# Performance work log

Hardware: AMD Instinct MI355X
Metric: run time of the kernel (lower is better)

Reference implementation:

```python
import jax, jax.numpy as jnp
import numpy as np

EMBED = 256
HEADS = 8
HD = EMBED // HEADS          # head_dim = key_dim = 32 (value_factor=1)
SCALE = HD ** (-0.5)


def angle_transform(x, sin, cos):
    # x: (b, nh, h, w, hd); sin/cos broadcast over leading dims
    x1 = x[..., ::2]
    x2 = x[..., 1::2]
    rot = jnp.stack([-x2, x1], axis=-1).reshape(x.shape)  # interleave (-x2, x1)
    return x * cos + rot * sin


def setup_inputs() -> dict:
    key = jax.random.key(0)
    ks = jax.random.split(key, 12)
    B, H, W = 4, 48, 48
    x = jax.random.normal(ks[0], (B, H, W, EMBED), jnp.float32)
    ang = jax.random.normal(ks[1], (H, W, HD), jnp.float32)
    sin = jnp.sin(ang)
    cos = jnp.cos(ang)
    mask = jax.random.normal(ks[2], (HEADS, H * W, H * W), jnp.float32) * 0.1
    s = 0.05
    Wq = jax.random.normal(ks[3], (EMBED, EMBED), jnp.float32) * s
    bq = jnp.zeros((EMBED,), jnp.float32)
    Wk = jax.random.normal(ks[4], (EMBED, EMBED), jnp.float32) * s
    bk = jnp.zeros((EMBED,), jnp.float32)
    Wv = jax.random.normal(ks[5], (EMBED, EMBED), jnp.float32) * s
    bv = jnp.zeros((EMBED,), jnp.float32)
    lepe_w = jax.random.normal(ks[6], (5, 5, 1, EMBED), jnp.float32) * 0.1  # HWIO, depthwise
    lepe_b = jnp.zeros((EMBED,), jnp.float32)
    Wout = jax.random.normal(ks[7], (EMBED, EMBED), jnp.float32) * s
    bout = jnp.zeros((EMBED,), jnp.float32)
    return {"x": x, "sin": sin, "cos": cos, "mask": mask,
            "Wq": Wq, "bq": bq, "Wk": Wk, "bk": bk, "Wv": Wv, "bv": bv,
            "lepe_w": lepe_w, "lepe_b": lepe_b, "Wout": Wout, "bout": bout}


def reference(x, sin, cos, mask, Wq, bq, Wk, bk, Wv, bv, lepe_w, lepe_b, Wout, bout):
    B, H, W, C = x.shape
    q = x @ Wq + bq
    k = (x @ Wk + bk) * SCALE
    v = x @ Wv + bv
    # depthwise 5x5 conv (lepe) on v, NHWC
    lepe = jax.lax.conv_general_dilated(
        v, lepe_w, window_strides=(1, 1), padding=[(2, 2), (2, 2)],
        dimension_numbers=("NHWC", "HWIO", "NHWC"), feature_group_count=C) + lepe_b
    qh = q.reshape(B, H, W, HEADS, HD).transpose(0, 3, 1, 2, 4)  # (b,nh,h,w,hd)
    kh = k.reshape(B, H, W, HEADS, HD).transpose(0, 3, 1, 2, 4)
    qr = angle_transform(qh, sin, cos).reshape(B, HEADS, H * W, HD)
    kr = angle_transform(kh, sin, cos).reshape(B, HEADS, H * W, HD)
    vr = v.reshape(B, H, W, HEADS, -1).transpose(0, 3, 1, 2, 4).reshape(B, HEADS, H * W, -1)
    attn = jax.nn.softmax(jnp.einsum("bnqd,bnkd->bnqk", qr, kr) + mask, axis=-1)
    out = jnp.einsum("bnqk,bnkd->bnqd", attn, vr)
    out = out.transpose(0, 2, 1, 3).reshape(B, H, W, -1) + lepe
    return out @ Wout + bout
```

## Files before the change

kernel.cpp:

```cpp
#include <hip/hip_runtime.h>
#include <hip/hip_bf16.h>
#include <math.h>

constexpr int kB     = 4;
constexpr int kH     = 48;
constexpr int kW     = 48;
constexpr int kHW    = 2304;
constexpr int kC     = 256;
constexpr int kHeads = 8;
constexpr int kHD    = 32;
constexpr float kScale = 0.17677669529663687f;

typedef __bf16 bf16x8 __attribute__((ext_vector_type(8)));
typedef float  f32x4  __attribute__((ext_vector_type(4)));
typedef unsigned int   uint32x4 __attribute__((ext_vector_type(4)));
typedef unsigned short ushort8v __attribute__((ext_vector_type(8)));

static __device__ __forceinline__ unsigned short f2bf_bits(float f) {
    return __builtin_bit_cast(unsigned short, __float2bfloat16(f));
}

static __device__ __forceinline__ unsigned cvt_pk_bf16(float lo, float hi) {
    unsigned r;
    asm("v_cvt_pk_bf16_f32 %0, %1, %2" : "=v"(r) : "v"(lo), "v"(hi));
    return r;
}

static __device__ __forceinline__ void gll16(const void* g, void* l) {
    __builtin_amdgcn_global_load_lds(
        (const __attribute__((address_space(1))) void*)g,
        (__attribute__((address_space(3))) void*)l, 16, 0, 0);
}

__global__ __launch_bounds__(256) void prep_kernel(
    const float* __restrict__ x,
    const float* __restrict__ Wq, const float* __restrict__ Wk,
    const float* __restrict__ Wv, const float* __restrict__ Wo,
    unsigned short* __restrict__ xb, unsigned short* __restrict__ wt)
{
    const int bid = blockIdx.x;
    if (bid < 2304) {
        const int i = (bid * 256 + threadIdx.x) * 4;
        const float4 v = *reinterpret_cast<const float4*>(x + i);
        alignas(8) unsigned short u[4] = {f2bf_bits(v.x), f2bf_bits(v.y),
                                          f2bf_bits(v.z), f2bf_bits(v.w)};
        *reinterpret_cast<unsigned long long*>(xb + i) =
            *reinterpret_cast<unsigned long long*>(u);
    } else {
        const int e = (bid - 2304) * 256 + threadIdx.x;
        const int m = e >> 16;
        const int r = e & 65535;
        const int k = r >> 8;
        const int n = r & 255;
        const float* W = (m == 0) ? Wq : ((m == 1) ? Wk : ((m == 2) ? Wv : Wo));
        wt[(size_t)m * 65536 + n * 256 + k] = f2bf_bits(W[k * 256 + n]);
    }
}

__global__ __launch_bounds__(256) void qkv_mfma_kernel(
    const unsigned short* __restrict__ xb, const unsigned short* __restrict__ wt,
    const float* __restrict__ bq, const float* __restrict__ bk,
    const float* __restrict__ bv,
    const float* __restrict__ sinb, const float* __restrict__ cosb,
    unsigned short* __restrict__ qbh, unsigned short* __restrict__ kbh,
    unsigned short* __restrict__ vt, float* __restrict__ vb)
{
    const int z = blockIdx.z;
    const unsigned short* wz = wt + (size_t)z * 65536;
    const float* bt = (z == 0) ? bq : ((z == 1) ? bk : bv);
    const int tid  = threadIdx.x;
    const int w    = tid >> 6;
    const int lane = tid & 63;
    const int l    = lane & 15;
    const int g    = lane >> 4;
    const int m0   = blockIdx.x * 64 + w * 16;
    const int nb   = blockIdx.y * 64;

    f32x4 acc[4] = {};
    const unsigned short* xrow = xb + (size_t)(m0 + l) * 256;
    #pragma unroll
    for (int kc = 0; kc < 8; ++kc) {
        const bf16x8 a = *reinterpret_cast<const bf16x8*>(xrow + kc * 32 + g * 8);
        #pragma unroll
        for (int j = 0; j < 4; ++j) {
            const bf16x8 b = *reinterpret_cast<const bf16x8*>(
                wz + (size_t)(nb + 16 * j + l) * 256 + kc * 32 + g * 8);
            acc[j] = __builtin_amdgcn_mfma_f32_16x16x32_bf16(a, b, acc[j], 0, 0, 0);
        }
    }

    int tok[4], bidx[4], hw[4];
    #pragma unroll
    for (int r = 0; r < 4; ++r) {
        tok[r]  = m0 + 4 * g + r;
        bidx[r] = tok[r] / kHW;
        hw[r]   = tok[r] - bidx[r] * kHW;
    }
    const float scl = (z == 1) ? kScale : 1.0f;

    if (z == 2) {
        #pragma unroll
        for (int j = 0; j < 4; ++j) {
            const int c = nb + 16 * j + l;
            const int head = c >> 5, d = c & 31;
            const float bias = bt[c];
            float t[4];
            #pragma unroll
            for (int r = 0; r < 4; ++r) t[r] = acc[j][r] + bias;
            #pragma unroll
            for (int r = 0; r < 4; ++r)
                vb[(((size_t)(bidx[r] * kHeads + head) * kHW + hw[r]) << 5) + d] = t[r];
            alignas(8) unsigned short u[4] = {f2bf_bits(t[0]), f2bf_bits(t[1]),
                                              f2bf_bits(t[2]), f2bf_bits(t[3])};
            *reinterpret_cast<unsigned long long*>(
                vt + ((size_t)(bidx[0] * kHeads + head) * kHD + d) * kHW + hw[0]) =
                *reinterpret_cast<unsigned long long*>(u);
        }
    } else {
        unsigned short* ob = (z == 0) ? qbh : kbh;
        #pragma unroll
        for (int j = 0; j < 4; ++j) {
            const int c = nb + 16 * j + l;
            const int head = c >> 5, d = c & 31;
            const float bias = bt[c];
            float t[4];
            #pragma unroll
            for (int r = 0; r < 4; ++r) t[r] = (acc[j][r] + bias) * scl;
            #pragma unroll
            for (int r = 0; r < 4; ++r) {
                const float p = __shfl_xor(t[r], 1);
                const float cs = cosb[hw[r] * 32 + d];
                const float sn = sinb[hw[r] * 32 + d];
                const float o = (d & 1) ? (t[r] * cs + p * sn)
                                        : (t[r] * cs - p * sn);
                ob[(((size_t)(bidx[r] * kHeads + head) * kHW + hw[r]) << 5) + d] =
                    f2bf_bits(o);
            }
        }
    }
}

__global__ __launch_bounds__(256) void lepe_kernel(
    const float* __restrict__ vb,
    const float* __restrict__ lw, const float* __restrict__ lb,
    float* __restrict__ lepe)
{
    const int c   = threadIdx.x;
    const int bhw = blockIdx.x;
    const int b   = bhw / kHW;
    const int hw  = bhw % kHW;
    const int h   = hw / kW;
    const int w   = hw % kW;
    const int head = c >> 5;
    const int d    = c & 31;

    const float* vsrc = vb + ((size_t)(b * kHeads + head) * kHW) * kHD + d;
    float acc = lb[c];
    #pragma unroll
    for (int dh = 0; dh < 5; ++dh) {
        const int h2 = h + dh - 2;
        if (h2 < 0 || h2 >= kH) continue;
        #pragma unroll
        for (int dw = 0; dw < 5; ++dw) {
            const int w2 = w + dw - 2;
            if (w2 < 0 || w2 >= kW) continue;
            acc += vsrc[(size_t)(h2 * kW + w2) * kHD] * lw[(dh * 5 + dw) * kC + c];
        }
    }
    lepe[(size_t)bhw * kC + c] = acc;
}

__global__ __launch_bounds__(512, 1) void attn_mfma_kernel(
    const __hip_bfloat16* __restrict__ qb, const __hip_bfloat16* __restrict__ kb,
    const __hip_bfloat16* __restrict__ vt, const float* __restrict__ mask,
    float* __restrict__ po, float* __restrict__ ls, int kspan)
{
    extern __shared__ __align__(16) char smem[];
    constexpr int kBufStride = 49152;
    constexpr int kKOff = 16384;
    constexpr int kVOff = 32768;

    const int head = blockIdx.y;
    const int ksl  = blockIdx.z;
    const int tid  = threadIdx.x;
    const int w    = tid >> 6;
    const int b    = w & 3;
    const int sh   = w >> 2;
    const int bh   = b * kHeads + head;
    const int lane = tid & 63;
    const int lq   = lane & 15;
    const int g    = lane >> 4;
    const int q0   = blockIdx.x * 64;
    const int kt0  = ksl * kspan;
    const int nt   = kspan >> 6;

    bf16x8 qfrag[2];
    #pragma unroll
    for (int si = 0; si < 2; ++si)
        qfrag[si] = *reinterpret_cast<const bf16x8*>(
            reinterpret_cast<const unsigned short*>(qb) +
            ((size_t)bh * kHW + q0 + 16 * (2 * sh + si) + lq) * kHD + g * 8);

    const float* msrc[2];
    #pragma unroll
    for (int i = 0; i < 2; ++i) {
        const int mrow = w * 8 + i * 4 + (lane >> 4);
        const int mcb  = (lane & 15) ^ (mrow & 7);
        msrc[i] = mask + ((size_t)head * kHW + q0 + mrow) * kHW + kt0 + mcb * 4;
    }
    const unsigned short* kvsrc[4];
    int kvstep, kvregion;
    {
        const unsigned short* kb_bh =
            reinterpret_cast<const unsigned short*>(kb) + (size_t)bh * kHW * kHD;
        const unsigned short* vt_bh =
            reinterpret_cast<const unsigned short*>(vt) + (size_t)bh * kHD * kHW;
        if (sh == 0) {
            #pragma unroll
            for (int i = 0; i < 4; ++i) {
                const int key   = i * 16 + (lane >> 2);
                const int kslot = (lane & 3) ^ (key & 3);
                kvsrc[i] = kb_bh + (size_t)(kt0 + key) * kHD + kslot * 8;
            }
            kvstep = 64 * kHD;
            kvregion = kKOff;
        } else {
            #pragma unroll
            for (int i = 0; i < 4; ++i) {
                const int d   = i * 8 + (lane >> 3);
                const int vcu = (lane & 7) ^ (d & 7);
                kvsrc[i] = vt_bh + (size_t)d * kHW + kt0 + vcu * 8;
            }
            kvstep = 64;
            kvregion = kVOff;
        }
    }

    auto STAGE = [&](int bufo, int tt) {
        char* mb = smem + bufo;
        #pragma unroll
        for (int i = 0; i < 2; ++i)
            gll16(msrc[i] + (size_t)tt * 64, mb + (w * 8 + i * 4) * 256);
        char* kv = smem + bufo + kvregion + b * 4096;
        #pragma unroll
        for (int i = 0; i < 4; ++i)
            gll16(kvsrc[i] + (size_t)tt * kvstep, kv + i * 1024);
    };

    f32x4 o0[2] = {};
    f32x4 o1[2] = {};
    float lsum[2] = {};
    const bool ghi = (g >= 2);

    const int koff = lq * 64 + ((g ^ (lq & 3)) * 16);
    const int vxa  = (g ^ (lq & 7)) * 16;
    const int vxb  = ((4 + g) ^ (lq & 7)) * 16;

    STAGE(0, 0);

    int cur = 0;
    for (int t = 0; t < nt; ++t) {
        if (t + 1 < nt) {
            STAGE(cur ^ kBufStride, t + 1);
            asm volatile("s_waitcnt vmcnt(6)" ::: "memory");
        } else {
            asm volatile("s_waitcnt vmcnt(0)" ::: "memory");
        }
        __builtin_amdgcn_s_barrier();
        __builtin_amdgcn_sched_barrier(0);

        const char* mb  = smem + cur;
        const char* kbf = smem + cur + kKOff + b * 4096;
        const char* vbf = smem + cur + kVOff + b * 4096;

        bf16x8 kf[4];
        #pragma unroll
        for (int j = 0; j < 4; ++j)
            kf[j] = *reinterpret_cast<const bf16x8*>(kbf + j * 1024 + koff);
        const bf16x8 va  = *reinterpret_cast<const bf16x8*>(vbf + lq * 128 + vxa);
        const bf16x8 vb2 = *reinterpret_cast<const bf16x8*>(vbf + lq * 128 + vxb);
        const bf16x8 vc  = *reinterpret_cast<const bf16x8*>(vbf + (16 + lq) * 128 + vxa);
        const bf16x8 vd  = *reinterpret_cast<const bf16x8*>(vbf + (16 + lq) * 128 + vxb);

        #pragma unroll
        for (int si = 0; si < 2; ++si) {
            const int s = 2 * sh + si;
            f32x4 st[4];
            #pragma unroll
            for (int j = 0; j < 4; ++j) {
                const f32x4 mc = *reinterpret_cast<const f32x4*>(
                    mb + s * 4096 + lq * 256 + (((4 * j + g) ^ (lq & 7)) * 16));
                st[j] = __builtin_amdgcn_mfma_f32_16x16x32_bf16(kf[j], qfrag[si], mc, 0, 0, 0);
            }

            unsigned p32[4][2];
            #pragma unroll
            for (int j = 0; j < 4; ++j) {
                const float e0 = __expf(st[j][0]);
                const float e1 = __expf(st[j][1]);
                const float e2 = __expf(st[j][2]);
                const float e3 = __expf(st[j][3]);
                lsum[si] += (e0 + e1) + (e2 + e3);
                p32[j][0] = cvt_pk_bf16(e0, e1);
                p32[j][1] = cvt_pk_bf16(e2, e3);
            }

            unsigned pw0[4], pw1[4];
            #pragma unroll
            for (int t2 = 0; t2 < 4; ++t2) {
                const int src = lq + 16 * (2 * (g & 1) + (t2 >> 1));
                const unsigned a0 = __shfl(p32[0][t2 & 1], src);
                const unsigned a1 = __shfl(p32[1][t2 & 1], src);
                const unsigned b0 = __shfl(p32[2][t2 & 1], src);
                const unsigned b1 = __shfl(p32[3][t2 & 1], src);
                pw0[t2] = ghi ? a1 : a0;
                pw1[t2] = ghi ? b1 : b0;
            }
            uint32x4 w0 = {pw0[0], pw0[1], pw0[2], pw0[3]};
            uint32x4 w1 = {pw1[0], pw1[1], pw1[2], pw1[3]};
            const bf16x8 pa0 = __builtin_bit_cast(bf16x8, w0);
            const bf16x8 pa1 = __builtin_bit_cast(bf16x8, w1);

            o0[si] = __builtin_amdgcn_mfma_f32_16x16x32_bf16(pa0, va,  o0[si], 0, 0, 0);
            o0[si] = __builtin_amdgcn_mfma_f32_16x16x32_bf16(pa1, vb2, o0[si], 0, 0, 0);
            o1[si] = __builtin_amdgcn_mfma_f32_16x16x32_bf16(pa0, vc,  o1[si], 0, 0, 0);
            o1[si] = __builtin_amdgcn_mfma_f32_16x16x32_bf16(pa1, vd,  o1[si], 0, 0, 0);
        }

        asm volatile("s_waitcnt lgkmcnt(0)" ::: "memory");
        __builtin_amdgcn_s_barrier();
        cur ^= kBufStride;
    }

    const size_t pbase = ((size_t)ksl * (kB * kHeads) + bh) * kHW;
    #pragma unroll
    for (int si = 0; si < 2; ++si) {
        const int s = 2 * sh + si;
        float l = lsum[si];
        l += __shfl_xor(l, 16);
        l += __shfl_xor(l, 32);
        #pragma unroll
        for (int r = 0; r < 4; ++r) {
            float* orow = po + (pbase + q0 + 16 * s + 4 * g + r) * kHD + lq;
            orow[0]  = o0[si][r];
            orow[16] = o1[si][r];
        }
        if (lane < 16) ls[pbase + q0 + 16 * s + lq] = l;
    }
}

__global__ __launch_bounds__(256) void combine_kernel(
    const float* __restrict__ po, const float* __restrict__ ls,
    const float* __restrict__ lepe, unsigned short* __restrict__ abh, int ks)
{
    const int idx = blockIdx.x * 256 + threadIdx.x;
    const int c   = idx & 255;
    const int bhw = idx >> 8;
    const int b   = bhw / kHW;
    const int hw  = bhw % kHW;
    const int head = c >> 5;
    const int d    = c & 31;
    const int bh   = b * kHeads + head;

    float o = 0.f, l = 0.f;
    for (int s = 0; s < ks; ++s) {
        const size_t pbase = ((size_t)s * (kB * kHeads) + bh) * kHW + hw;
        o += po[pbase * kHD + d];
        l += ls[pbase];
    }
    abh[(size_t)idx] = f2bf_bits(o / l + lepe[idx]);
}

__global__ __launch_bounds__(256) void out_mfma_kernel(
    const unsigned short* __restrict__ abh, const unsigned short* __restrict__ wt,
    const float* __restrict__ bo, float* __restrict__ out)
{
    const unsigned short* wz = wt + (size_t)3 * 65536;
    const int tid  = threadIdx.x;
    const int w    = tid >> 6;
    const int lane = tid & 63;
    const int l    = lane & 15;
    const int g    = lane >> 4;
    const int m0   = blockIdx.x * 64 + w * 16;
    const int nb   = blockIdx.y * 64;

    f32x4 acc[4] = {};
    const unsigned short* arow = abh + (size_t)(m0 + l) * 256;
    #pragma unroll
    for (int kc = 0; kc < 8; ++kc) {
        const bf16x8 a = *reinterpret_cast<const bf16x8*>(arow + kc * 32 + g * 8);
        #pragma unroll
        for (int j = 0; j < 4; ++j) {
            const bf16x8 b = *reinterpret_cast<const bf16x8*>(
                wz + (size_t)(nb + 16 * j + l) * 256 + kc * 32 + g * 8);
            acc[j] = __builtin_amdgcn_mfma_f32_16x16x32_bf16(a, b, acc[j], 0, 0, 0);
        }
    }

    #pragma unroll
    for (int j = 0; j < 4; ++j) {
        const int c = nb + 16 * j + l;
        const float bias = bo[c];
        #pragma unroll
        for (int r = 0; r < 4; ++r)
            out[(size_t)(m0 + 4 * g + r) * 256 + c] = acc[j][r] + bias;
    }
}

extern "C" void kernel_launch(void* const* d_in, const int* in_sizes, int n_in,
                              void* d_out, int out_size, void* d_ws, size_t ws_size,
                              hipStream_t stream)
{
    const float* x    = (const float*)d_in[0];
    const float* sinb = (const float*)d_in[1];
    const float* cosb = (const float*)d_in[2];
    const float* mask = (const float*)d_in[3];
    const float* Wq   = (const float*)d_in[4];
    const float* bq   = (const float*)d_in[5];
    const float* Wk   = (const float*)d_in[6];
    const float* bk   = (const float*)d_in[7];
    const float* Wv   = (const float*)d_in[8];
    const float* bv   = (const float*)d_in[9];
    const float* lw   = (const float*)d_in[10];
    const float* lb   = (const float*)d_in[11];
    const float* Wo   = (const float*)d_in[12];
    const float* bo   = (const float*)d_in[13];
    float* out = (float*)d_out;

    const size_t NT = (size_t)kB * kHeads * kHW * kHD;
    const size_t fixed = NT * 4 * 2 + NT * 2 * 5 + 4 * 65536 * 2;

    int ks = 4;
    while (ks > 1) {
        const size_t need = fixed + (size_t)ks * (NT * 4 + (size_t)kB * kHeads * kHW * 4);
        if (need <= ws_size) break;
        ks >>= 1;
    }
    const int kspan = kHW / ks;

    char* base = (char*)d_ws;
    float* vb   = (float*)base;                      base += NT * 4;
    float* lepe = (float*)base;                      base += NT * 4;
    unsigned short* xb  = (unsigned short*)base;     base += NT * 2;
    unsigned short* abh = (unsigned short*)base;     base += NT * 2;
    unsigned short* qbh = (unsigned short*)base;     base += NT * 2;
    unsigned short* kbh = (unsigned short*)base;     base += NT * 2;
    unsigned short* vt  = (unsigned short*)base;     base += NT * 2;
    unsigned short* wt  = (unsigned short*)base;     base += (size_t)4 * 65536 * 2;
    float* po = (float*)base;                        base += (size_t)ks * NT * 4;
    float* ls = (float*)base;                        base += (size_t)ks * kB * kHeads * kHW * 4;

    prep_kernel<<<dim3(3328), 256, 0, stream>>>(x, Wq, Wk, Wv, Wo, xb, wt);
    qkv_mfma_kernel<<<dim3(144, 4, 3), 256, 0, stream>>>(
        xb, wt, bq, bk, bv, sinb, cosb, qbh, kbh, vt, vb);
    lepe_kernel<<<dim3(9216), 256, 0, stream>>>(vb, lw, lb, lepe);
    attn_mfma_kernel<<<dim3(36, 8, ks), 512, 98304, stream>>>(
        (const __hip_bfloat16*)qbh, (const __hip_bfloat16*)kbh,
        (const __hip_bfloat16*)vt, mask, po, ls, kspan);
    combine_kernel<<<dim3(9216), 256, 0, stream>>>(po, ls, lepe, abh, ks);
    out_mfma_kernel<<<dim3(144, 4), 256, 0, stream>>>(abh, wt, bo, out);
}
```

Before: 208.8 us.

## Halve attention query tile and swap shuffles for permlane swaps

The attention kernel now handles 32 queries per block instead of 64. Each wave holds one 16-row query slice, and the grid doubles to 72 blocks along x. Shared memory per block drops, and launch bounds ask for 4 blocks per CU, to raise occupancy and improve latency hiding on the mask stream. The bf16 P-matrix transposition between the two MFMAs now uses v_permlane16/32_swap instead of ds_bpermute-based __shfl, which cuts LDS traffic. The cost is that K/V tiles are reloaded twice as often per query, since each block reuses them across fewer queries.

```diff
diff --git a/kernel.cpp b/kernel.cpp
--- a/kernel.cpp
+++ b/kernel.cpp
@@ -24,6 +24,13 @@
     unsigned r;
     asm("v_cvt_pk_bf16_f32 %0, %1, %2" : "=v"(r) : "v"(lo), "v"(hi));
     return r;
+}
+
+static __device__ __forceinline__ void permlane16_swap(unsigned& a, unsigned& b) {
+    asm("v_permlane16_swap_b32 %0, %1" : "+v"(a), "+v"(b));
+}
+static __device__ __forceinline__ void permlane32_swap(unsigned& a, unsigned& b) {
+    asm("v_permlane32_swap_b32 %0, %1" : "+v"(a), "+v"(b));
 }
 
 static __device__ __forceinline__ void gll16(const void* g, void* l) {
@@ -170,15 +177,15 @@
     lepe[(size_t)bhw * kC + c] = acc;
 }
 
-__global__ __launch_bounds__(512, 1) void attn_mfma_kernel(
+__global__ __launch_bounds__(512, 4) void attn_mfma_kernel(
     const __hip_bfloat16* __restrict__ qb, const __hip_bfloat16* __restrict__ kb,
     const __hip_bfloat16* __restrict__ vt, const float* __restrict__ mask,
     float* __restrict__ po, float* __restrict__ ls, int kspan)
 {
     extern __shared__ __align__(16) char smem[];
-    constexpr int kBufStride = 49152;
-    constexpr int kKOff = 16384;
-    constexpr int kVOff = 32768;
+    constexpr int kBufStride = 40960;
+    constexpr int kKOff = 8192;
+    constexpr int kVOff = 24576;
 
     const int head = blockIdx.y;
     const int ksl  = blockIdx.z;
@@ -190,23 +197,20 @@
     const int lane = tid & 63;
     const int lq   = lane & 15;
     const int g    = lane >> 4;
-    const int q0   = blockIdx.x * 64;
+    const int q0   = blockIdx.x * 32;
     const int kt0  = ksl * kspan;
     const int nt   = kspan >> 6;
-
-    bf16x8 qfrag[2];
-    #pragma unroll
-    for (int si = 0; si < 2; ++si)
-        qfrag[si] = *reinterpret_cast<const bf16x8*>(
-            reinterpret_cast<const unsigned short*>(qb) +
-            ((size_t)bh * kHW + q0 + 16 * (2 * sh + si) + lq) * kHD + g * 8);
-
-    const float* msrc[2];
-    #pragma unroll
-    for (int i = 0; i < 2; ++i) {
-        const int mrow = w * 8 + i * 4 + (lane >> 4);
+    const bool odd16 = (g & 1);
+
+    const bf16x8 qfrag = *reinterpret_cast<const bf16x8*>(
+        reinterpret_cast<const unsigned short*>(qb) +
+        ((size_t)bh * kHW + q0 + 16 * sh + lq) * kHD + g * 8);
+
+    const float* msrc;
+    {
+        const int mrow = w * 4 + (lane >> 4);
         const int mcb  = (lane & 15) ^ (mrow & 7);
-        msrc[i] = mask + ((size_t)head * kHW + q0 + mrow) * kHW + kt0 + mcb * 4;
+        msrc = mask + ((size_t)head * kHW + q0 + mrow) * kHW + kt0 + mcb * 4;
     }
     const unsigned short* kvsrc[4];
     int kvstep, kvregion;
@@ -237,20 +241,16 @@
     }
 
     auto STAGE = [&](int bufo, int tt) {
-        char* mb = smem + bufo;
-        #pragma unroll
-        for (int i = 0; i < 2; ++i)
-            gll16(msrc[i] + (size_t)tt * 64, mb + (w * 8 + i * 4) * 256);
+        gll16(msrc + (size_t)tt * 64, smem + bufo + w * 1024);
         char* kv = smem + bufo + kvregion + b * 4096;
         #pragma unroll
         for (int i = 0; i < 4; ++i)
             gll16(kvsrc[i] + (size_t)tt * kvstep, kv + i * 1024);
     };
 
-    f32x4 o0[2] = {};
-    f32x4 o1[2] = {};
-    float lsum[2] = {};
-    const bool ghi = (g >= 2);
+    f32x4 o0 = {0.f, 0.f, 0.f, 0.f};
+    f32x4 o1 = {0.f, 0.f, 0.f, 0.f};
+    float lsum = 0.f;
 
     const int koff = lq * 64 + ((g ^ (lq & 3)) * 16);
     const int vxa  = (g ^ (lq & 7)) * 16;
@@ -262,7 +262,7 @@
     for (int t = 0; t < nt; ++t) {
         if (t + 1 < nt) {
             STAGE(cur ^ kBufStride, t + 1);
-            asm volatile("s_waitcnt vmcnt(6)" ::: "memory");
+            asm volatile("s_waitcnt vmcnt(5)" ::: "memory");
         } else {
             asm volatile("s_waitcnt vmcnt(0)" ::: "memory");
         }
@@ -282,71 +282,72 @@
         const bf16x8 vc  = *reinterpret_cast<const bf16x8*>(vbf + (16 + lq) * 128 + vxa);
         const bf16x8 vd  = *reinterpret_cast<const bf16x8*>(vbf + (16 + lq) * 128 + vxb);
 
-        #pragma unroll
-        for (int si = 0; si < 2; ++si) {
-            const int s = 2 * sh + si;
-            f32x4 st[4];
-            #pragma unroll
-            for (int j = 0; j < 4; ++j) {
-                const f32x4 mc = *reinterpret_cast<const f32x4*>(
-                    mb + s * 4096 + lq * 256 + (((4 * j + g) ^ (lq & 7)) * 16));
-                st[j] = __builtin_amdgcn_mfma_f32_16x16x32_bf16(kf[j], qfrag[si], mc, 0, 0, 0);
+        f32x4 st[4];
+        #pragma unroll
+        for (int j = 0; j < 4; ++j) {
+            const f32x4 mc = *reinterpret_cast<const f32x4*>(
+                mb + sh * 4096 + lq * 256 + (((4 * j + g) ^ (lq & 7)) * 16));
+            st[j] = __builtin_amdgcn_mfma_f32_16x16x32_bf16(kf[j], qfrag, mc, 0, 0, 0);
+        }
+
+        unsigned p32[4][2];
+        #pragma unroll
+        for (int j = 0; j < 4; ++j) {
+            const float e0 = __expf(st[j][0]);
+            const float e1 = __expf(st[j][1]);
+            const float e2 = __expf(st[j][2]);
+            const float e3 = __expf(st[j][3]);
+            lsum += (e0 + e1) + (e2 + e3);
+            p32[j][0] = cvt_pk_bf16(e0, e1);
+            p32[j][1] = cvt_pk_bf16(e2, e3);
+        }
+
+        unsigned sj[4][2][2];
+        #pragma unroll
+        for (int j = 0; j < 4; ++j)
+            #pragma unroll
+            for (int r = 0; r < 2; ++r) {
+                unsigned a = p32[j][r], b2 = p32[j][r];
+                permlane16_swap(a, b2);
+                sj[j][r][0] = a; sj[j][r][1] = b2;
             }
-
-            unsigned p32[4][2];
-            #pragma unroll
-            for (int j = 0; j < 4; ++j) {
-                const float e0 = __expf(st[j][0]);
-                const float e1 = __expf(st[j][1]);
-                const float e2 = __expf(st[j][2]);
-                const float e3 = __expf(st[j][3]);
-                lsum[si] += (e0 + e1) + (e2 + e3);
-                p32[j][0] = cvt_pk_bf16(e0, e1);
-                p32[j][1] = cvt_pk_bf16(e2, e3);
-            }
-
-            unsigned pw0[4], pw1[4];
-            #pragma unroll
-            for (int t2 = 0; t2 < 4; ++t2) {
-                const int src = lq + 16 * (2 * (g & 1) + (t2 >> 1));
-                const unsigned a0 = __shfl(p32[0][t2 & 1], src);
-                const unsigned a1 = __shfl(p32[1][t2 & 1], src);
-                const unsigned b0 = __shfl(p32[2][t2 & 1], src);
-                const unsigned b1 = __shfl(p32[3][t2 & 1], src);
-                pw0[t2] = ghi ? a1 : a0;
-                pw1[t2] = ghi ? b1 : b0;
-            }
-            uint32x4 w0 = {pw0[0], pw0[1], pw0[2], pw0[3]};
-            uint32x4 w1 = {pw1[0], pw1[1], pw1[2], pw1[3]};
-            const bf16x8 pa0 = __builtin_bit_cast(bf16x8, w0);
-            const bf16x8 pa1 = __builtin_bit_cast(bf16x8, w1);
-
-            o0[si] = __builtin_amdgcn_mfma_f32_16x16x32_bf16(pa0, va,  o0[si], 0, 0, 0);
-            o0[si] = __builtin_amdgcn_mfma_f32_16x16x32_bf16(pa1, vb2, o0[si], 0, 0, 0);
-            o1[si] = __builtin_amdgcn_mfma_f32_16x16x32_bf16(pa0, vc,  o1[si], 0, 0, 0);
-            o1[si] = __builtin_amdgcn_mfma_f32_16x16x32_bf16(pa1, vd,  o1[si], 0, 0, 0);
-        }
+        unsigned pw0[4], pw1[4];
+        #pragma unroll
+        for (int w2 = 0; w2 < 4; ++w2) {
+            const int r = w2 & 1, c = w2 >> 1;
+            unsigned pa = sj[0][r][c], pb = sj[1][r][c];
+            permlane32_swap(pa, pb);
+            pw0[w2] = odd16 ? pb : pa;
+            unsigned qa = sj[2][r][c], qb2 = sj[3][r][c];
+            permlane32_swap(qa, qb2);
+            pw1[w2] = odd16 ? qb2 : qa;
+        }
+        uint32x4 w0v = {pw0[0], pw0[1], pw0[2], pw0[3]};
+        uint32x4 w1v = {pw1[0], pw1[1], pw1[2], pw1[3]};
+        const bf16x8 pa0 = __builtin_bit_cast(bf16x8, w0v);
+        const bf16x8 pa1 = __builtin_bit_cast(bf16x8, w1v);
+
+        o0 = __builtin_amdgcn_mfma_f32_16x16x32_bf16(pa0, va,  o0, 0, 0, 0);
+        o0 = __builtin_amdgcn_mfma_f32_16x16x32_bf16(pa1, vb2, o0, 0, 0, 0);
+        o1 = __builtin_amdgcn_mfma_f32_16x16x32_bf16(pa0, vc,  o1, 0, 0, 0);
+        o1 = __builtin_amdgcn_mfma_f32_16x16x32_bf16(pa1, vd,  o1, 0, 0, 0);
 
         asm volatile("s_waitcnt lgkmcnt(0)" ::: "memory");
         __builtin_amdgcn_s_barrier();
         cur ^= kBufStride;
     }
 
+    lsum += __shfl_xor(lsum, 16);
+    lsum += __shfl_xor(lsum, 32);
+
     const size_t pbase = ((size_t)ksl * (kB * kHeads) + bh) * kHW;
     #pragma unroll
-    for (int si = 0; si < 2; ++si) {
-        const int s = 2 * sh + si;
-        float l = lsum[si];
-        l += __shfl_xor(l, 16);
-        l += __shfl_xor(l, 32);
-        #pragma unroll
-        for (int r = 0; r < 4; ++r) {
-            float* orow = po + (pbase + q0 + 16 * s + 4 * g + r) * kHD + lq;
-            orow[0]  = o0[si][r];
-            orow[16] = o1[si][r];
-        }
-        if (lane < 16) ls[pbase + q0 + 16 * s + lq] = l;
-    }
+    for (int r = 0; r < 4; ++r) {
+        float* orow = po + (pbase + q0 + 16 * sh + 4 * g + r) * kHD + lq;
+        orow[0]  = o0[r];
+        orow[16] = o1[r];
+    }
+    if (lane < 16) ls[pbase + q0 + 16 * sh + lq] = lsum;
 }
 
 __global__ __launch_bounds__(256) void combine_kernel(
@@ -454,7 +455,7 @@
     qkv_mfma_kernel<<<dim3(144, 4, 3), 256, 0, stream>>>(
         xb, wt, bq, bk, bv, sinb, cosb, qbh, kbh, vt, vb);
     lepe_kernel<<<dim3(9216), 256, 0, stream>>>(vb, lw, lb, lepe);
-    attn_mfma_kernel<<<dim3(36, 8, ks), 512, 98304, stream>>>(
+    attn_mfma_kernel<<<dim3(72, 8, ks), 512, 81920, stream>>>(
         (const __hip_bfloat16*)qbh, (const __hip_bfloat16*)kbh,
         (const __hip_bfloat16*)vt, mask, po, ls, kspan);
     combine_kernel<<<dim3(9216), 256, 0, stream>>>(po, ls, lepe, abh, ks);
```

Result: faster. 186.5 us, median of 3 (-10.7%).
